# Kernel optimization log

Measured on AMD Instinct MI355X. Metric: run time of the kernel, lower is better.

Reference implementation:

```python
import jax, jax.numpy as jnp
import numpy as np

B, P, E, S = 4, 2048, 4096, 16


def setup_inputs() -> dict:
    key = jax.random.key(0)
    ks = jax.random.split(key, 6)
    return {
        "x": jax.random.normal(ks[0], (B, P, E), dtype=jnp.float32),
        "product": jax.random.normal(ks[1], (P, S), dtype=jnp.float32) * 0.1,
        "person": jax.random.normal(ks[2], (E, S), dtype=jnp.float32) * 0.1,
        "W1": jax.random.normal(ks[3], (2 * S, S), dtype=jnp.float32) * (1.0 / np.sqrt(2 * S)),
        "W2": jax.random.normal(ks[4], (S, S), dtype=jnp.float32) * (1.0 / np.sqrt(S)),
        "W3": jax.random.normal(ks[5], (S, 1), dtype=jnp.float32) * (1.0 / np.sqrt(S)),
    }


def reference(x, product, person, W1, W2, W3):
    # cartesian product concat([pr, pe]) @ W1 == pr @ W1[:S] + pe @ W1[S:]
    # (no bias), so we avoid materializing the (P*E, 2S) concat tensor.
    Wa, Wb = W1[:S], W1[S:]           # each (S, S)
    h1 = jnp.tanh(
        (product @ Wa)[:, None, :] +  # (P, 1, S)
        (person @ Wb)[None, :, :]     # (1, E, S)
    )                                  # (P, E, S)
    h2 = jnp.tanh(h1 @ W2)            # (P, E, S)
    z = (h2 @ W3)[..., 0]             # (P, E)
    score = jnp.where(z >= 0, z, 0.1 * z)  # leaky relu, alpha=0.1
    return score[None, :, :] * x      # (B, P, E)
```

## Files before the change

### kernel.cpp

```cpp
#include <hip/hip_runtime.h>

#define BB 4
#define PP 2048
#define EE 4096
#define SS 16

static __device__ __forceinline__ float fast_exp2(float x) {
#if __has_builtin(__builtin_amdgcn_exp2f)
    return __builtin_amdgcn_exp2f(x);
#else
    return exp2f(x);
#endif
}

static __device__ __forceinline__ float fast_tanh(float x) {
    float xc = fminf(fmaxf(x, -9.0f), 9.0f);
    float t  = fast_exp2(xc * 2.885390081777927f);
    return (t - 1.0f) * __builtin_amdgcn_rcpf(t + 1.0f);
}

__global__ __launch_bounds__(256) void precompute_ab(
    const float* __restrict__ product, const float* __restrict__ person,
    const float* __restrict__ W1, float* __restrict__ a, float* __restrict__ b)
{
    int row = blockIdx.x * blockDim.x + threadIdx.x;
    if (row >= PP + EE) return;
    const bool  is_p  = row < PP;
    const float* in   = is_p ? (product + (size_t)row * SS)
                             : (person  + (size_t)(row - PP) * SS);
    const float* W    = is_p ? W1 : (W1 + SS * SS);
    float*       orow = is_p ? (a + (size_t)row * SS)
                             : (b + (size_t)(row - PP) * SS);
    float v[SS];
#pragma unroll
    for (int k = 0; k < SS; ++k) v[k] = in[k];
#pragma unroll
    for (int j = 0; j < SS; ++j) {
        float acc = 0.0f;
#pragma unroll
        for (int k = 0; k < SS; ++k) acc = fmaf(v[k], W[k * SS + j], acc);
        orow[j] = acc;
    }
}

__global__ __launch_bounds__(256) void score_mul(
    const float* __restrict__ x, const float* __restrict__ a,
    const float* __restrict__ b, const float* __restrict__ W2,
    const float* __restrict__ W3, float* __restrict__ out)
{
    const int p = blockIdx.y;
    const int e = blockIdx.x * 256 + threadIdx.x;

    const float4* brow = (const float4*)(b + (size_t)e * SS);
    float4 b0 = brow[0], b1 = brow[1], b2 = brow[2], b3 = brow[3];
    float br[SS] = {b0.x,b0.y,b0.z,b0.w, b1.x,b1.y,b1.z,b1.w,
                    b2.x,b2.y,b2.z,b2.w, b3.x,b3.y,b3.z,b3.w};

    float h1[SS];
#pragma unroll
    for (int s = 0; s < SS; ++s) h1[s] = fast_tanh(a[(size_t)p * SS + s] + br[s]);

    float acc[SS];
#pragma unroll
    for (int j = 0; j < SS; ++j) acc[j] = 0.0f;
#pragma unroll
    for (int s = 0; s < SS; ++s) {
#pragma unroll
        for (int j = 0; j < SS; ++j)
            acc[j] = fmaf(h1[s], W2[s * SS + j], acc[j]);
    }

    float z = 0.0f;
#pragma unroll
    for (int j = 0; j < SS; ++j) z = fmaf(fast_tanh(acc[j]), W3[j], z);
    float score = (z >= 0.0f) ? z : 0.1f * z;

    const size_t base = (size_t)p * EE + (size_t)e;
#pragma unroll
    for (int bb = 0; bb < BB; ++bb) {
        const size_t idx = (size_t)bb * ((size_t)PP * EE) + base;
        out[idx] = score * x[idx];
    }
}

extern "C" void kernel_launch(void* const* d_in, const int* in_sizes, int n_in,
                              void* d_out, int out_size, void* d_ws, size_t ws_size,
                              hipStream_t stream)
{
    const float* x       = (const float*)d_in[0];
    const float* product = (const float*)d_in[1];
    const float* person  = (const float*)d_in[2];
    const float* W1      = (const float*)d_in[3];
    const float* W2      = (const float*)d_in[4];
    const float* W3      = (const float*)d_in[5];
    float* out = (float*)d_out;

    float* a = (float*)d_ws;
    float* b = a + (size_t)PP * SS;

    dim3 g1((PP + EE + 255) / 256);
    precompute_ab<<<g1, 256, 0, stream>>>(product, person, W1, a, b);

    dim3 g2(EE / 256, PP);
    score_mul<<<g2, 256, 0, stream>>>(x, a, b, W2, W3, out);
}
```

Measured before the change: 294.1 us.

## Compute W2 layer with fp16 MFMA and tile 16 products per block

Replaces the per-thread 16x16 FMA matmul for the second layer with fp16 MFMA instructions. h1 is packed to half precision and staged through shared memory to form the B fragments. Each block now processes 16 product rows, reusing its person row and W2/W3 fragments, and x loads are issued before compute. This reduces ALU work, at the cost of reduced precision in the W2 product.

```diff
diff --git a/kernel.cpp b/kernel.cpp
--- a/kernel.cpp
+++ b/kernel.cpp
@@ -4,18 +4,16 @@
 #define PP 2048
 #define EE 4096
 #define SS 16
+#define TP 16
+#define EBLK 256
 
-static __device__ __forceinline__ float fast_exp2(float x) {
-#if __has_builtin(__builtin_amdgcn_exp2f)
-    return __builtin_amdgcn_exp2f(x);
-#else
-    return exp2f(x);
-#endif
-}
+typedef __fp16 v2h __attribute__((ext_vector_type(2)));
+typedef __fp16 v4h __attribute__((ext_vector_type(4)));
+typedef float  v4f __attribute__((ext_vector_type(4)));
 
 static __device__ __forceinline__ float fast_tanh(float x) {
     float xc = fminf(fmaxf(x, -9.0f), 9.0f);
-    float t  = fast_exp2(xc * 2.885390081777927f);
+    float t  = __builtin_amdgcn_exp2f(xc * 2.885390081777927f);
     return (t - 1.0f) * __builtin_amdgcn_rcpf(t + 1.0f);
 }
 
@@ -43,43 +41,97 @@
     }
 }
 
-__global__ __launch_bounds__(256) void score_mul(
+__global__ __launch_bounds__(256, 4) void score_mul(
     const float* __restrict__ x, const float* __restrict__ a,
     const float* __restrict__ b, const float* __restrict__ W2,
     const float* __restrict__ W3, float* __restrict__ out)
 {
-    const int p = blockIdx.y;
-    const int e = blockIdx.x * 256 + threadIdx.x;
+    const int tid  = threadIdx.x;
+    const int lane = tid & 63;
+    const int wv   = tid >> 6;
+    const int n    = lane & 15;
+    const int q    = lane >> 4;
 
-    const float4* brow = (const float4*)(b + (size_t)e * SS);
-    float4 b0 = brow[0], b1 = brow[1], b2 = brow[2], b3 = brow[3];
-    float br[SS] = {b0.x,b0.y,b0.z,b0.w, b1.x,b1.y,b1.z,b1.w,
-                    b2.x,b2.y,b2.z,b2.w, b3.x,b3.y,b3.z,b3.w};
+    const int e  = blockIdx.x * EBLK + tid;
+    const int p0 = blockIdx.y * TP;
 
-    float h1[SS];
+    __shared__ int h1s[4][64][8];
+
+    float br[SS];
+    {
+        const float4* brp = (const float4*)(b + (size_t)e * SS);
 #pragma unroll
-    for (int s = 0; s < SS; ++s) h1[s] = fast_tanh(a[(size_t)p * SS + s] + br[s]);
-
-    float acc[SS];
-#pragma unroll
-    for (int j = 0; j < SS; ++j) acc[j] = 0.0f;
-#pragma unroll
-    for (int s = 0; s < SS; ++s) {
-#pragma unroll
-        for (int j = 0; j < SS; ++j)
-            acc[j] = fmaf(h1[s], W2[s * SS + j], acc[j]);
+        for (int i = 0; i < 4; ++i) {
+            float4 t = brp[i];
+            br[4*i+0]=t.x; br[4*i+1]=t.y; br[4*i+2]=t.z; br[4*i+3]=t.w;
+        }
     }
 
-    float z = 0.0f;
+    v4h w2a;
+    {
+        float c0 = W2[(q*4+0)*SS + n];
+        float c1 = W2[(q*4+1)*SS + n];
+        float c2 = W2[(q*4+2)*SS + n];
+        float c3 = W2[(q*4+3)*SS + n];
+        v2h lo = __builtin_amdgcn_cvt_pkrtz(c0, c1);
+        v2h hi = __builtin_amdgcn_cvt_pkrtz(c2, c3);
+        w2a[0]=lo[0]; w2a[1]=lo[1]; w2a[2]=hi[0]; w2a[3]=hi[1];
+    }
+
+    float4 w3v = ((const float4*)W3)[q];
+    const float w3r[4] = {w3v.x, w3v.y, w3v.z, w3v.w};
+
+    for (int ip = 0; ip < TP; ++ip) {
+        const int p = p0 + ip;
+        const size_t base = (size_t)p * EE + (size_t)e;
+
+        float xv[BB];
 #pragma unroll
-    for (int j = 0; j < SS; ++j) z = fmaf(fast_tanh(acc[j]), W3[j], z);
-    float score = (z >= 0.0f) ? z : 0.1f * z;
+        for (int bb2 = 0; bb2 < BB; ++bb2)
+            xv[bb2] = x[(size_t)bb2 * ((size_t)PP * EE) + base];
 
-    const size_t base = (size_t)p * EE + (size_t)e;
+        const float* __restrict__ ap = a + (size_t)p * SS;
+        int hp[8];
 #pragma unroll
-    for (int bb = 0; bb < BB; ++bb) {
-        const size_t idx = (size_t)bb * ((size_t)PP * EE) + base;
-        out[idx] = score * x[idx];
+        for (int r = 0; r < 8; ++r) {
+            float t0 = fast_tanh(ap[2*r+0] + br[2*r+0]);
+            float t1 = fast_tanh(ap[2*r+1] + br[2*r+1]);
+            hp[r] = __builtin_bit_cast(int, __builtin_amdgcn_cvt_pkrtz(t0, t1));
+        }
+
+        int* myrow = &h1s[wv][lane][0];
+        *(int4*)(myrow + 0) = make_int4(hp[0], hp[1], hp[2], hp[3]);
+        *(int4*)(myrow + 4) = make_int4(hp[4], hp[5], hp[6], hp[7]);
+        __builtin_amdgcn_wave_barrier();
+
+        v4f acc[4];
+#pragma unroll
+        for (int g = 0; g < 4; ++g) {
+            int2 rb = *(const int2*)&h1s[wv][g*16 + n][q*2];
+            v4h bfrag = __builtin_bit_cast(v4h, rb);
+            v4f z4 = {0.f, 0.f, 0.f, 0.f};
+            acc[g] = __builtin_amdgcn_mfma_f32_16x16x16f16(w2a, bfrag, z4, 0, 0, 0);
+        }
+
+        float pg[4];
+#pragma unroll
+        for (int g = 0; g < 4; ++g) {
+            float s = 0.f;
+#pragma unroll
+            for (int r = 0; r < 4; ++r)
+                s = fmaf(fast_tanh(acc[g][r]), w3r[r], s);
+            s += __shfl_xor(s, 16);
+            s += __shfl_xor(s, 32);
+            pg[g] = s;
+        }
+        float s01 = (q & 1) ? pg[1] : pg[0];
+        float s23 = (q & 1) ? pg[3] : pg[2];
+        float z   = (q & 2) ? s23 : s01;
+        float sc  = fmaxf(z, 0.f) + 0.1f * fminf(z, 0.f);
+
+#pragma unroll
+        for (int bb2 = 0; bb2 < BB; ++bb2)
+            out[(size_t)bb2 * ((size_t)PP * EE) + base] = sc * xv[bb2];
     }
 }
 
@@ -101,6 +153,6 @@
     dim3 g1((PP + EE + 255) / 256);
     precompute_ab<<<g1, 256, 0, stream>>>(product, person, W1, a, b);
 
-    dim3 g2(EE / 256, PP);
+    dim3 g2(EE / EBLK, PP / TP);
     score_mul<<<g2, 256, 0, stream>>>(x, a, b, W2, W3, out);
 }
```

Result: faster. 266.8 us (-9.3%).
